# Optimization experiments

Measured on AMD Instinct MI355X. Metric: run time of the kernel, lower is better.

Reference implementation:

```python
import jax, jax.numpy as jnp
import numpy as np

EPS = 1e-5


def _conv1x1(x, w, b):
    # x: (B,C,H,W), w: (O,C), b: (O,)
    return jnp.einsum('bchw,oc->bohw', x, w) + b[None, :, None, None]


def setup_inputs() -> dict:
    key = jax.random.key(0)
    ks = jax.random.split(key, 12)
    C, Ci = 512, 256
    B, H, W = 4, 64, 64
    s_in = 1.0 / np.sqrt(C)
    s_ci = 1.0 / np.sqrt(Ci)
    return {
        'x': jax.random.normal(ks[0], (B, C, H, W), dtype=jnp.float32),
        'g_w': jax.random.normal(ks[1], (Ci, C), dtype=jnp.float32) * s_in,
        'g_b': jax.random.normal(ks[2], (Ci,), dtype=jnp.float32) * 0.01,
        'theta_w': jax.random.normal(ks[3], (Ci, C), dtype=jnp.float32) * s_in,
        'theta_b': jax.random.normal(ks[4], (Ci,), dtype=jnp.float32) * 0.01,
        'phi_w': jax.random.normal(ks[5], (Ci, C), dtype=jnp.float32) * s_in,
        'phi_b': jax.random.normal(ks[6], (Ci,), dtype=jnp.float32) * 0.01,
        'W_w': jax.random.normal(ks[7], (C, Ci), dtype=jnp.float32) * s_ci,
        'W_b': jax.random.normal(ks[8], (C,), dtype=jnp.float32) * 0.01,
        'bn_gamma': jax.random.normal(ks[9], (C,), dtype=jnp.float32) * 0.1,
        'bn_beta': jax.random.normal(ks[10], (C,), dtype=jnp.float32) * 0.01,
    }


def reference(x, g_w, g_b, theta_w, theta_b, phi_w, phi_b, W_w, W_b, bn_gamma, bn_beta):
    B, C, H, W = x.shape
    Ci = g_w.shape[0]
    HW = H * W
    # 1x1-conv projections -> token form
    g = _conv1x1(x, g_w, g_b).reshape(B, Ci, HW).transpose(0, 2, 1)        # (B,HW,Ci)
    theta = _conv1x1(x, theta_w, theta_b).reshape(B, Ci, HW).transpose(0, 2, 1)  # (B,HW,Ci)
    phi = _conv1x1(x, phi_w, phi_b).reshape(B, Ci, HW)                      # (B,Ci,HW)
    # dense HWxHW attention, scaled by sqrt(inter_channels)
    pairwise = jnp.einsum('bnc,bcm->bnm', theta, phi) / jnp.sqrt(jnp.float32(Ci))
    attn = jax.nn.softmax(pairwise, axis=-1)
    y = jnp.einsum('bnm,bmc->bnc', attn, g)                                 # (B,HW,Ci)
    y = y.transpose(0, 2, 1).reshape(B, Ci, H, W)
    # output 1x1 conv + BatchNorm2d (training-mode batch statistics)
    z = _conv1x1(y, W_w, W_b)
    mean = jnp.mean(z, axis=(0, 2, 3), keepdims=True)
    var = jnp.var(z, axis=(0, 2, 3), keepdims=True)
    z = bn_gamma[None, :, None, None] * (z - mean) * jax.lax.rsqrt(var + EPS) + bn_beta[None, :, None, None]
    return z + x
```

## Files before the change

kernel.cpp:

```cpp
#include <hip/hip_runtime.h>

typedef unsigned short u16;
typedef __attribute__((ext_vector_type(4))) u16 u16x4;
typedef __attribute__((ext_vector_type(8))) u16 u16x8;
typedef __attribute__((ext_vector_type(8))) short s16x8;
typedef __attribute__((ext_vector_type(4))) float f32x4;
typedef __attribute__((ext_vector_type(16))) float f32x16;

#define B_  4
#define C_  512
#define CI_ 256
#define HW_ 4096

static __device__ __forceinline__ u16 f2bf(float f) {
  unsigned u = __float_as_uint(f);
  return (u16)((u + 0x7FFFu + ((u >> 16) & 1u)) >> 16);
}
static __device__ __forceinline__ float bf2f(u16 h) {
  return __uint_as_float(((unsigned)h) << 16);
}

static __device__ __forceinline__ f32x4 mfma16(s16x8 a, s16x8 b, f32x4 c) {
  return __builtin_amdgcn_mfma_f32_16x16x32_bf16(a, b, c, 0, 0, 0);
}
static __device__ __forceinline__ f32x16 mfma32(s16x8 a, s16x8 b, f32x16 c) {
  return __builtin_amdgcn_mfma_f32_32x32x16_bf16(a, b, c, 0, 0, 0);
}

typedef __attribute__((address_space(3))) unsigned int as3_u32;
typedef const __attribute__((address_space(1))) unsigned int as1_u32;
static __device__ __forceinline__ void gload16(const u16* g, u16* l) {
  __builtin_amdgcn_global_load_lds((as1_u32*)g, (as3_u32*)l, 16, 0, 0);
}

__global__ __launch_bounds__(256) void k0_wcvt(
    const float* __restrict__ wg, const float* __restrict__ wt,
    const float* __restrict__ wp, const float* __restrict__ Ww,
    u16* __restrict__ wB, u16* __restrict__ WwB)
{
  int idx = (blockIdx.x * 256 + threadIdx.x) * 8;
  const float* src;
  u16* dst;
  if (idx < 393216) {
    int r = idx >> 17;
    src = (r == 0 ? wg : r == 1 ? wt : wp) + (idx & 131071);
    dst = wB + idx;
  } else {
    src = Ww + (idx - 393216);
    dst = WwB + (idx - 393216);
  }
  float4 v0 = *reinterpret_cast<const float4*>(src);
  float4 v1 = *reinterpret_cast<const float4*>(src + 4);
  u16x8 h;
  h[0] = f2bf(v0.x); h[1] = f2bf(v0.y); h[2] = f2bf(v0.z); h[3] = f2bf(v0.w);
  h[4] = f2bf(v1.x); h[5] = f2bf(v1.y); h[6] = f2bf(v1.z); h[7] = f2bf(v1.w);
  *reinterpret_cast<u16x8*>(dst) = h;
}

__global__ __launch_bounds__(256) void k0_xt(
    const float* __restrict__ x, u16* __restrict__ xT, int b0)
{
  __shared__ u16 lds[64][72];
  const int tid = threadIdx.x;
  const int n0 = blockIdx.x * 64, c0 = blockIdx.y * 64;
  const int bl = blockIdx.z;
  const int b = b0 + bl;
  const int nc = (tid & 15) * 4;
#pragma unroll
  for (int i = 0; i < 4; ++i) {
    int cr = (tid >> 4) + i * 16;
    float4 v = *reinterpret_cast<const float4*>(
        &x[((size_t)(b * C_ + c0 + cr)) * HW_ + n0 + nc]);
    u16x4 h; h[0] = f2bf(v.x); h[1] = f2bf(v.y); h[2] = f2bf(v.z); h[3] = f2bf(v.w);
    *reinterpret_cast<u16x4*>(&lds[cr][nc]) = h;
  }
  __syncthreads();
  const int n = tid & 63, cg = tid >> 6;
  u16x8 o0, o1;
#pragma unroll
  for (int j = 0; j < 8; ++j) { o0[j] = lds[cg * 16 + j][n]; o1[j] = lds[cg * 16 + 8 + j][n]; }
  size_t dstb = ((size_t)bl * HW_ + n0 + n) * C_ + c0 + cg * 16;
  *reinterpret_cast<u16x8*>(&xT[dstb])     = o0;
  *reinterpret_cast<u16x8*>(&xT[dstb + 8]) = o1;
}

__global__ __launch_bounds__(256) void k1_proj(
    const u16* __restrict__ wB, const u16* __restrict__ xT,
    const float* __restrict__ bg, const float* __restrict__ bt, const float* __restrict__ bp,
    u16* __restrict__ g_s, u16* __restrict__ thetaT, u16* __restrict__ phiT, int half)
{
  extern __shared__ u16 sm1[];
  const int tid = threadIdx.x;
  const int lane = tid & 63, wid = tid >> 6;
  const int wm = wid >> 1, wn = wid & 1;
  const int l15 = lane & 15, g4 = lane >> 4;

  const int bid = blockIdx.x;
  const int r12 = bid % 12;
  const int nt = bid / 12;
  const int mt = r12 >> 1;
  const int bl = r12 & 1;
  const int b = half * 2 + bl;
  const int m0 = mt * 128, n0g = nt * 128;
  const int p = mt >> 1;

  const u16* xb = xT + (size_t)bl * HW_ * C_;

  const int srow = tid >> 2, sch = tid & 3;
  const u16* a_src = wB + (size_t)(m0 + srow) * C_ + sch * 8;
  const u16* b_src = xb + (size_t)(n0g + srow) * C_ + sch * 8;

  f32x4 acc[4][4] = {};

  auto stage1 = [&](int buf, int ks) {
    u16* d = sm1 + buf * 8192;
#pragma unroll
    for (int i = 0; i < 2; ++i) {
      gload16(a_src + (size_t)(i * 64) * C_ + ks * 32, d + (tid + i * 256) * 8);
      gload16(b_src + (size_t)(i * 64) * C_ + ks * 32, d + 4096 + (tid + i * 256) * 8);
    }
  };
  auto compute1 = [&](int buf) {
    const u16* A = sm1 + buf * 8192;
    const u16* Bt = A + 4096;
    s16x8 afr[4], bfr[4];
#pragma unroll
    for (int mf = 0; mf < 4; ++mf)
      afr[mf] = *reinterpret_cast<const s16x8*>(&A[(wm * 64 + mf * 16 + l15) * 32 + g4 * 8]);
#pragma unroll
    for (int nf = 0; nf < 4; ++nf)
      bfr[nf] = *reinterpret_cast<const s16x8*>(&Bt[(wn * 64 + nf * 16 + l15) * 32 + g4 * 8]);
#pragma unroll
    for (int mf = 0; mf < 4; ++mf)
#pragma unroll
      for (int nf = 0; nf < 4; ++nf)
        acc[mf][nf] = mfma16(afr[mf], bfr[nf], acc[mf][nf]);
  };

  stage1(0, 0); stage1(1, 1);
  int cur = 0;
#pragma unroll 1
  for (int ks = 0; ks < 15; ++ks) {
    asm volatile("s_waitcnt vmcnt(4)" ::: "memory");
    __builtin_amdgcn_s_barrier();
    compute1(cur);
    if (ks < 14) { int nb = cur + 2; if (nb >= 3) nb -= 3; stage1(nb, ks + 2); }
    cur = (cur == 2) ? 0 : cur + 1;
  }
  asm volatile("s_waitcnt vmcnt(0)" ::: "memory");
  __builtin_amdgcn_s_barrier();
  compute1(cur);
  __syncthreads();

  const float* bias = (p == 0) ? bg : (p == 1) ? bt : bp;
  const int cib = (mt & 1) * 128;
#pragma unroll
  for (int mf = 0; mf < 4; ++mf)
#pragma unroll
    for (int r = 0; r < 4; ++r) {
      float bv = bias[cib + wm * 64 + mf * 16 + g4 * 4 + r];
#pragma unroll
      for (int nf = 0; nf < 4; ++nf) acc[mf][nf][r] += bv;
    }

  if (p == 0) {
    u16* lds_t = sm1;
#pragma unroll
    for (int mf = 0; mf < 4; ++mf)
#pragma unroll
      for (int nf = 0; nf < 4; ++nf)
#pragma unroll
        for (int r = 0; r < 4; ++r)
          lds_t[(wm * 64 + mf * 16 + g4 * 4 + r) * 136 + wn * 64 + nf * 16 + l15] =
              f2bf(acc[mf][nf][r]);
    __syncthreads();
    const int m = tid >> 1, hh = tid & 1;
    size_t dst = ((size_t)b * CI_ + cib + m) * HW_ + n0g + hh * 64;
#pragma unroll
    for (int j = 0; j < 8; ++j)
      *reinterpret_cast<u16x8*>(&g_s[dst + j * 8]) =
          *reinterpret_cast<const u16x8*>(&lds_t[m * 136 + hh * 64 + j * 8]);
  } else {
    u16* outp = (p == 1) ? thetaT : phiT;
#pragma unroll
    for (int mf = 0; mf < 4; ++mf)
#pragma unroll
      for (int nf = 0; nf < 4; ++nf) {
        u16x4 h;
#pragma unroll
        for (int r = 0; r < 4; ++r) h[r] = f2bf(acc[mf][nf][r]);
        int n = n0g + wn * 64 + nf * 16 + l15;
        *reinterpret_cast<u16x4*>(
            &outp[((size_t)b * HW_ + n) * CI_ + cib + wm * 64 + mf * 16 + g4 * 4]) = h;
      }
  }
}

#define OFF_PHI  0
#define OFF_G    32768
#define OFF_P    65536
#define OFF_LP   73728

__global__ __launch_bounds__(512, 2) void k3_fused(
    const u16* __restrict__ thetaT, const u16* __restrict__ phiT,
    const u16* __restrict__ g_s, u16* __restrict__ y)
{
  extern __shared__ u16 smem[];
  float* Lp = (float*)(smem + OFF_LP);
  float* iL = Lp + 256;

  const int tid = threadIdx.x;
  const int lane = tid & 63, w = tid >> 6;
  const int l31 = lane & 31, h = lane >> 5;
  const int l15 = lane & 15;

  const int bid = blockIdx.x;
  const int xcd = bid & 7, slot = bid >> 3;
  const int b  = xcd >> 1;
  const int n0 = ((xcd & 1) * 32 + slot) * 64;

  const int mh = w >> 1, nh = w & 1;
  const int cq = w >> 1, nh2 = w & 1;

  const u16* thb = thetaT + (size_t)b * HW_ * CI_;
  const u16* phb = phiT   + (size_t)b * HW_ * CI_;
  const u16* gsb = g_s    + (size_t)b * CI_ * HW_;

  s16x8 thfr[16];
#pragma unroll
  for (int cs = 0; cs < 16; ++cs)
    thfr[cs] = *reinterpret_cast<const s16x8*>(
        &thb[(size_t)(n0 + nh * 32 + l31) * CI_ + cs * 16 + h * 8]);

  const int prow = tid >> 5, pj = tid & 31;
  const int grow = tid >> 4, gj = tid & 15;
  const u16* ph_src = phb + (size_t)prow * CI_ + ((pj ^ prow) * 8);
  const u16* g_src  = gsb + (size_t)grow * HW_ + ((gj ^ (grow & 15)) * 8);
  const int ph_do = prow * 256 + pj * 8;
  const int g_do  = grow * 128 + gj * 8;

  auto stage_phi = [&](int mt) {
#pragma unroll
    for (int i = 0; i < 8; ++i)
      gload16(ph_src + (size_t)(mt + i * 16) * CI_, smem + OFF_PHI + ph_do + i * 4096);
  };
  auto stage_g = [&](int mt) {
#pragma unroll
    for (int i = 0; i < 8; ++i)
      gload16(g_src + mt + (size_t)(i * 32) * HW_, smem + OFF_G + g_do + i * 4096);
  };

  f32x16 oacc[2] = {};
  float psum = 0.f;

  auto qk_it = [&]() {
    const u16* phc = smem + OFF_PHI;
    u16* pb = smem + OFF_P;
    f32x16 acc = {};
    __builtin_amdgcn_s_setprio(1);
#pragma unroll
    for (int cs = 0; cs < 16; ++cs) {
      s16x8 a = *reinterpret_cast<const s16x8*>(
          &phc[(mh * 32 + l31) * 256 + (((cs * 2 + h) ^ l15) * 8)]);
      acc = mfma32(a, thfr[cs], acc);
    }
    __builtin_amdgcn_s_setprio(0);
    const int nloc = nh * 32 + l31;
#pragma unroll
    for (int g = 0; g < 4; ++g) {
      u16x4 pk;
#pragma unroll
      for (int r = 0; r < 4; ++r) {
        float e = __expf(acc[4 * g + r] * 0.0625f);
        psum += e;
        pk[r] = f2bf(e);
      }
      *reinterpret_cast<u16x4*>(
          &pb[nloc * 128 + (((mh * 4 + g) ^ l15) * 8) + h * 4]) = pk;
    }
  };
  auto pv_it = [&]() {
    const u16* pb = smem + OFF_P;
    const u16* gC = smem + OFF_G;
    const int nloc = nh2 * 32 + l31;
    __builtin_amdgcn_s_setprio(1);
#pragma unroll
    for (int ks = 0; ks < 8; ++ks) {
      s16x8 pa = *reinterpret_cast<const s16x8*>(
          &pb[nloc * 128 + (((ks * 2 + h) ^ l15) * 8)]);
#pragma unroll
      for (int ct = 0; ct < 2; ++ct) {
        int c = cq * 64 + ct * 32 + l31;
        s16x8 gb = *reinterpret_cast<const s16x8*>(
            &gC[c * 128 + (((ks * 2 + h) ^ l15) * 8)]);
        oacc[ct] = mfma32(pa, gb, oacc[ct]);
      }
    }
    __builtin_amdgcn_s_setprio(0);
  };

  stage_phi(0);
  __syncthreads();

#pragma unroll 1
  for (int it = 0; it < 32; ++it) {
    stage_g(it * 128);
    qk_it();
    __syncthreads();
    if (it < 31) stage_phi((it + 1) * 128);
    pv_it();
    __syncthreads();
  }

  psum += __shfl_xor(psum, 32);
  if (lane < 32) Lp[w * 32 + lane] = psum;
  __syncthreads();
  if (tid < 64) {
    int nhh = tid >> 5, j = tid & 31;
    iL[tid] = 1.0f / (Lp[(0 * 2 + nhh) * 32 + j] + Lp[(1 * 2 + nhh) * 32 + j] +
                      Lp[(2 * 2 + nhh) * 32 + j] + Lp[(3 * 2 + nhh) * 32 + j]);
  }
  __syncthreads();

  u16* yb = y + ((size_t)b * HW_ + n0) * CI_;
#pragma unroll
  for (int ct = 0; ct < 2; ++ct) {
    int c = cq * 64 + ct * 32 + l31;
#pragma unroll
    for (int reg = 0; reg < 16; ++reg) {
      int nl = nh2 * 32 + (reg & 3) + 8 * (reg >> 2) + 4 * h;
      yb[(size_t)nl * CI_ + c] = f2bf(oacc[ct][reg] * iL[nl]);
    }
  }
}

__global__ __launch_bounds__(256) void k4_wconv(
    const u16* __restrict__ WwB, const u16* __restrict__ y, const float* __restrict__ Wb,
    u16* __restrict__ z, float* __restrict__ zsum, float* __restrict__ zsq)
{
  extern __shared__ u16 sm4[];
  __shared__ float lds_ps[2][128][2];
  const int tid = threadIdx.x;
  const int lane = tid & 63, wid = tid >> 6;
  const int wm = wid >> 1, wn = wid & 1;
  const int l15 = lane & 15, g4 = lane >> 4;

  const int bid = blockIdx.x;
  const int xcd = bid & 7, slot = bid >> 3;
  const int b = xcd >> 1, half = xcd & 1;
  const int mt = slot & 3;
  const int nt = half * 16 + (slot >> 2);
  const int o0 = mt * 128, n0g = nt * 128;

  const int srow = tid >> 2, sch = tid & 3;
  const u16* a_src = WwB + (size_t)(o0 + srow) * CI_ + sch * 8;
  const u16* b_src = y + ((size_t)(b * HW_ + n0g + srow)) * CI_ + sch * 8;

  f32x4 acc[4][4] = {};

  auto stage4 = [&](int buf, int ks) {
    u16* d = sm4 + buf * 8192;
#pragma unroll
    for (int i = 0; i < 2; ++i) {
      gload16(a_src + (size_t)(i * 64) * CI_ + ks * 32, d + (tid + i * 256) * 8);
      gload16(b_src + (size_t)(i * 64) * CI_ + ks * 32, d + 4096 + (tid + i * 256) * 8);
    }
  };
  auto compute4 = [&](int buf) {
    const u16* A = sm4 + buf * 8192;
    const u16* Bt = A + 4096;
    s16x8 afr[4], bfr[4];
#pragma unroll
    for (int mf = 0; mf < 4; ++mf)
      afr[mf] = *reinterpret_cast<const s16x8*>(&A[(wm * 64 + mf * 16 + l15) * 32 + g4 * 8]);
#pragma unroll
    for (int nf = 0; nf < 4; ++nf)
      bfr[nf] = *reinterpret_cast<const s16x8*>(&Bt[(wn * 64 + nf * 16 + l15) * 32 + g4 * 8]);
#pragma unroll
    for (int mf = 0; mf < 4; ++mf)
#pragma unroll
      for (int nf = 0; nf < 4; ++nf)
        acc[mf][nf] = mfma16(afr[mf], bfr[nf], acc[mf][nf]);
  };

  stage4(0, 0); stage4(1, 1);
  int cur = 0;
#pragma unroll 1
  for (int ks = 0; ks < 7; ++ks) {
    asm volatile("s_waitcnt vmcnt(4)" ::: "memory");
    __builtin_amdgcn_s_barrier();
    compute4(cur);
    if (ks < 6) { int nb = cur + 2; if (nb >= 3) nb -= 3; stage4(nb, ks + 2); }
    cur = (cur == 2) ? 0 : cur + 1;
  }
  asm volatile("s_waitcnt vmcnt(0)" ::: "memory");
  __builtin_amdgcn_s_barrier();
  compute4(cur);
  __syncthreads();

  u16* lds_t = sm4;
#pragma unroll
  for (int mf = 0; mf < 4; ++mf)
#pragma unroll
    for (int r = 0; r < 4; ++r) {
      const int ol = wm * 64 + mf * 16 + g4 * 4 + r;
      float wb = Wb[o0 + ol];
      float s = 0.f, q = 0.f;
#pragma unroll
      for (int nf = 0; nf < 4; ++nf) {
        float zv = acc[mf][nf][r] + wb;
        s += zv; q += zv * zv;
        lds_t[ol * 136 + wn * 64 + nf * 16 + l15] = f2bf(zv);
      }
      s += __shfl_xor(s, 1); s += __shfl_xor(s, 2); s += __shfl_xor(s, 4); s += __shfl_xor(s, 8);
      q += __shfl_xor(q, 1); q += __shfl_xor(q, 2); q += __shfl_xor(q, 4); q += __shfl_xor(q, 8);
      if (l15 == 0) { lds_ps[wn][ol][0] = s; lds_ps[wn][ol][1] = q; }
    }
  __syncthreads();
  {
    const int m = tid >> 1, hh = tid & 1;
    size_t dst = ((size_t)(b * C_ + o0 + m)) * HW_ + n0g + hh * 64;
#pragma unroll
    for (int j = 0; j < 8; ++j)
      *reinterpret_cast<u16x8*>(&z[dst + j * 8]) =
          *reinterpret_cast<const u16x8*>(&lds_t[m * 136 + hh * 64 + j * 8]);
  }
  if (tid < 128) {
    int col = b * 32 + nt;
    zsum[(size_t)(o0 + tid) * 128 + col] = lds_ps[0][tid][0] + lds_ps[1][tid][0];
    zsq [(size_t)(o0 + tid) * 128 + col] = lds_ps[0][tid][1] + lds_ps[1][tid][1];
  }
}

__global__ void k5_bnstat(const float* __restrict__ zsum, const float* __restrict__ zsq,
                          const float* __restrict__ gamma, const float* __restrict__ beta,
                          float* __restrict__ bns, float* __restrict__ bnb)
{
  int ch = blockIdx.x * 256 + threadIdx.x;
  if (ch >= C_) return;
  float s = 0.f, q = 0.f;
  for (int i = 0; i < 128; ++i) { s += zsum[(size_t)ch * 128 + i]; q += zsq[(size_t)ch * 128 + i]; }
  const float inv_n = 1.0f / (B_ * HW_);
  float mean = s * inv_n;
  float var  = q * inv_n - mean * mean;
  float sc = gamma[ch] * rsqrtf(var + 1e-5f);
  bns[ch] = sc;
  bnb[ch] = beta[ch] - mean * sc;
}

__global__ __launch_bounds__(256) void k6_final(
    const u16* __restrict__ z, const float* __restrict__ x,
    const float* __restrict__ bns, const float* __restrict__ bnb,
    float* __restrict__ out)
{
  size_t i = ((size_t)blockIdx.x * 256 + threadIdx.x) * 8;
  int ch = (int)((i >> 12) & 511);
  float sc = bns[ch], sh = bnb[ch];
  u16x8 zv = *reinterpret_cast<const u16x8*>(&z[i]);
  float4 x0 = *reinterpret_cast<const float4*>(&x[i]);
  float4 x1 = *reinterpret_cast<const float4*>(&x[i + 4]);
  float4 o0, o1;
  o0.x = bf2f(zv[0]) * sc + sh + x0.x;
  o0.y = bf2f(zv[1]) * sc + sh + x0.y;
  o0.z = bf2f(zv[2]) * sc + sh + x0.z;
  o0.w = bf2f(zv[3]) * sc + sh + x0.w;
  o1.x = bf2f(zv[4]) * sc + sh + x1.x;
  o1.y = bf2f(zv[5]) * sc + sh + x1.y;
  o1.z = bf2f(zv[6]) * sc + sh + x1.z;
  o1.w = bf2f(zv[7]) * sc + sh + x1.w;
  *reinterpret_cast<float4*>(&out[i])     = o0;
  *reinterpret_cast<float4*>(&out[i + 4]) = o1;
}

extern "C" void kernel_launch(void* const* d_in, const int* in_sizes, int n_in,
                              void* d_out, int out_size, void* d_ws, size_t ws_size,
                              hipStream_t stream)
{
  (void)in_sizes; (void)n_in; (void)out_size; (void)ws_size;
  const float* x    = (const float*)d_in[0];
  const float* g_w  = (const float*)d_in[1];
  const float* g_b  = (const float*)d_in[2];
  const float* t_w  = (const float*)d_in[3];
  const float* t_b  = (const float*)d_in[4];
  const float* p_w  = (const float*)d_in[5];
  const float* p_b  = (const float*)d_in[6];
  const float* W_w  = (const float*)d_in[7];
  const float* W_b  = (const float*)d_in[8];
  const float* bng  = (const float*)d_in[9];
  const float* bnb_ = (const float*)d_in[10];

  char* ws = (char*)d_ws;
  const size_t M8 = (size_t)8 << 20;
  u16*   xT     = (u16*)(ws + 0);
  u16*   y      = (u16*)(ws + 0);
  u16*   thetaT = (u16*)(ws + M8);
  u16*   phiT   = (u16*)(ws + 2 * M8);
  u16*   g_s    = (u16*)(ws + 3 * M8);
  u16*   zbf    = (u16*)(ws + M8);
  float* zsum   = (float*)(ws + 3 * M8);
  float* zsq    = (float*)(ws + 3 * M8 + 262144);
  float* bnsV   = (float*)(ws + 3 * M8 + 524288);
  float* bnbV   = (float*)(ws + 3 * M8 + 526336);
  u16*   wB     = (u16*)(ws + 4 * M8);
  u16*   WwB    = (u16*)(ws + 4 * M8 + 786432);
  float* out    = (float*)d_out;

  const int k1_lds = 49152;
  const int k3_lds = 148736;
  const int k4_lds = 49152;
  hipFuncSetAttribute(reinterpret_cast<const void*>(k1_proj),
                      hipFuncAttributeMaxDynamicSharedMemorySize, k1_lds);
  hipFuncSetAttribute(reinterpret_cast<const void*>(k3_fused),
                      hipFuncAttributeMaxDynamicSharedMemorySize, k3_lds);
  hipFuncSetAttribute(reinterpret_cast<const void*>(k4_wconv),
                      hipFuncAttributeMaxDynamicSharedMemorySize, k4_lds);

  hipLaunchKernelGGL(k0_wcvt, dim3(256), dim3(256), 0, stream,
                     g_w, t_w, p_w, W_w, wB, WwB);
  for (int half = 0; half < 2; ++half) {
    hipLaunchKernelGGL(k0_xt, dim3(64, 8, 2), dim3(256), 0, stream, x, xT, half * 2);
    hipLaunchKernelGGL(k1_proj, dim3(384), dim3(256), k1_lds, stream,
                       wB, xT, g_b, t_b, p_b, g_s, thetaT, phiT, half);
  }
  hipLaunchKernelGGL(k3_fused, dim3(256), dim3(512), k3_lds, stream,
                     thetaT, phiT, g_s, y);
  hipLaunchKernelGGL(k4_wconv, dim3(512), dim3(256), k4_lds, stream,
                     WwB, y, W_b, zbf, zsum, zsq);
  hipLaunchKernelGGL(k5_bnstat, dim3(2), dim3(256), 0, stream,
                     zsum, zsq, bng, bnb_, bnsV, bnbV);
  hipLaunchKernelGGL(k6_final, dim3(4096), dim3(256), 0, stream,
                     zbf, x, bnsV, bnbV, out);
}
```

Before: 187.5 us.

## Keep softmax probabilities in registers and split PV over key slices

The attention kernel no longer writes exp-scores to an LDS P buffer for the PV matmul. Each wave packs its own QK accumulator into MFMA A-operands using lane shuffles. It then multiplies them against all 256 output channels for its slice of keys, which requires 8 f32x16 accumulators per wave. A serialized four-step LDS reduction across the key-slice waves follows, then vectorized bf16 stores. This removes the P write/read round-trip and a sync dependency, at the cost of much higher register pressure and an extra reduction phase.

```diff
diff --git a/kernel.cpp b/kernel.cpp
--- a/kernel.cpp
+++ b/kernel.cpp
@@ -6,6 +6,7 @@
 typedef __attribute__((ext_vector_type(8))) short s16x8;
 typedef __attribute__((ext_vector_type(4))) float f32x4;
 typedef __attribute__((ext_vector_type(16))) float f32x16;
+typedef __attribute__((ext_vector_type(4))) unsigned u32x4;
 
 #define B_  4
 #define C_  512
@@ -198,15 +199,14 @@
 
 #define OFF_PHI  0
 #define OFF_G    32768
-#define OFF_P    65536
-#define OFF_LP   73728
+#define OFF_LPW  65536
 
 __global__ __launch_bounds__(512, 2) void k3_fused(
     const u16* __restrict__ thetaT, const u16* __restrict__ phiT,
     const u16* __restrict__ g_s, u16* __restrict__ y)
 {
   extern __shared__ u16 smem[];
-  float* Lp = (float*)(smem + OFF_LP);
+  float* Lp = (float*)(smem + OFF_LPW);
   float* iL = Lp + 256;
 
   const int tid = threadIdx.x;
@@ -220,7 +220,6 @@
   const int n0 = ((xcd & 1) * 32 + slot) * 64;
 
   const int mh = w >> 1, nh = w & 1;
-  const int cq = w >> 1, nh2 = w & 1;
 
   const u16* thb = thetaT + (size_t)b * HW_ * CI_;
   const u16* phb = phiT   + (size_t)b * HW_ * CI_;
@@ -250,12 +249,12 @@
       gload16(g_src + mt + (size_t)(i * 32) * HW_, smem + OFF_G + g_do + i * 4096);
   };
 
-  f32x16 oacc[2] = {};
+  f32x16 oacc[8] = {};
   float psum = 0.f;
+  s16x8 pa0, pa1;
 
   auto qk_it = [&]() {
     const u16* phc = smem + OFF_PHI;
-    u16* pb = smem + OFF_P;
     f32x16 acc = {};
     __builtin_amdgcn_s_setprio(1);
 #pragma unroll
@@ -265,34 +264,50 @@
       acc = mfma32(a, thfr[cs], acc);
     }
     __builtin_amdgcn_s_setprio(0);
-    const int nloc = nh * 32 + l31;
-#pragma unroll
-    for (int g = 0; g < 4; ++g) {
-      u16x4 pk;
-#pragma unroll
-      for (int r = 0; r < 4; ++r) {
-        float e = __expf(acc[4 * g + r] * 0.0625f);
-        psum += e;
-        pk[r] = f2bf(e);
-      }
-      *reinterpret_cast<u16x4*>(
-          &pb[nloc * 128 + (((mh * 4 + g) ^ l15) * 8) + h * 4]) = pk;
-    }
-  };
+    float p[16];
+#pragma unroll
+    for (int r = 0; r < 16; ++r) {
+      p[r] = __expf(acc[r] * 0.0625f);
+      psum += p[r];
+    }
+    unsigned q[4][2];
+#pragma unroll
+    for (int qi = 0; qi < 4; ++qi) {
+      q[qi][0] = ((unsigned)f2bf(p[4 * qi + 1]) << 16) | f2bf(p[4 * qi]);
+      q[qi][1] = ((unsigned)f2bf(p[4 * qi + 3]) << 16) | f2bf(p[4 * qi + 2]);
+    }
+    unsigned sa0 = h ? q[0][0] : q[1][0];
+    unsigned sa1 = h ? q[0][1] : q[1][1];
+    unsigned sb0 = h ? q[2][0] : q[3][0];
+    unsigned sb1 = h ? q[2][1] : q[3][1];
+    unsigned ra0 = __shfl_xor(sa0, 32);
+    unsigned ra1 = __shfl_xor(sa1, 32);
+    unsigned rb0 = __shfl_xor(sb0, 32);
+    unsigned rb1 = __shfl_xor(sb1, 32);
+    u32x4 w0, w1;
+    w0[0] = h ? ra0 : q[0][0];
+    w0[1] = h ? ra1 : q[0][1];
+    w0[2] = h ? q[1][0] : ra0;
+    w0[3] = h ? q[1][1] : ra1;
+    w1[0] = h ? rb0 : q[2][0];
+    w1[1] = h ? rb1 : q[2][1];
+    w1[2] = h ? q[3][0] : rb0;
+    w1[3] = h ? q[3][1] : rb1;
+    pa0 = *reinterpret_cast<s16x8*>(&w0);
+    pa1 = *reinterpret_cast<s16x8*>(&w1);
+  };
+
   auto pv_it = [&]() {
-    const u16* pb = smem + OFF_P;
     const u16* gC = smem + OFF_G;
-    const int nloc = nh2 * 32 + l31;
     __builtin_amdgcn_s_setprio(1);
 #pragma unroll
-    for (int ks = 0; ks < 8; ++ks) {
-      s16x8 pa = *reinterpret_cast<const s16x8*>(
-          &pb[nloc * 128 + (((ks * 2 + h) ^ l15) * 8)]);
-#pragma unroll
-      for (int ct = 0; ct < 2; ++ct) {
-        int c = cq * 64 + ct * 32 + l31;
+    for (int ks = 0; ks < 2; ++ks) {
+      s16x8 pa = ks ? pa1 : pa0;
+      const int chunk = mh * 4 + ks * 2 + h;
+#pragma unroll
+      for (int ct = 0; ct < 8; ++ct) {
         s16x8 gb = *reinterpret_cast<const s16x8*>(
-            &gC[c * 128 + (((ks * 2 + h) ^ l15) * 8)]);
+            &gC[(ct * 32 + l31) * 128 + ((chunk ^ l15) * 8)]);
         oacc[ct] = mfma32(pa, gb, oacc[ct]);
       }
     }
@@ -322,14 +337,37 @@
   }
   __syncthreads();
 
+  float* ored = (float*)smem;
+#pragma unroll 1
+  for (int step = 0; step < 4; ++step) {
+    if (mh == step) {
+#pragma unroll
+      for (int ct = 0; ct < 8; ++ct)
+#pragma unroll
+        for (int reg = 0; reg < 16; ++reg) {
+          int n = nh * 32 + (reg & 3) + 8 * (reg >> 2) + 4 * h;
+          int c = ct * 32 + l31;
+          if (step == 0) ored[n * 260 + c] = oacc[ct][reg];
+          else           ored[n * 260 + c] += oacc[ct][reg];
+        }
+    }
+    __syncthreads();
+  }
+
   u16* yb = y + ((size_t)b * HW_ + n0) * CI_;
-#pragma unroll
-  for (int ct = 0; ct < 2; ++ct) {
-    int c = cq * 64 + ct * 32 + l31;
-#pragma unroll
-    for (int reg = 0; reg < 16; ++reg) {
-      int nl = nh2 * 32 + (reg & 3) + 8 * (reg >> 2) + 4 * h;
-      yb[(size_t)nl * CI_ + c] = f2bf(oacc[ct][reg] * iL[nl]);
+  {
+    const int n = tid >> 3, cc = (tid & 7) * 32;
+    float il = iL[n];
+#pragma unroll
+    for (int jj = 0; jj < 4; ++jj) {
+      f32x4 v0 = *reinterpret_cast<const f32x4*>(&ored[n * 260 + cc + jj * 8]);
+      f32x4 v1 = *reinterpret_cast<const f32x4*>(&ored[n * 260 + cc + jj * 8 + 4]);
+      u16x8 o;
+      o[0] = f2bf(v0[0] * il); o[1] = f2bf(v0[1] * il);
+      o[2] = f2bf(v0[2] * il); o[3] = f2bf(v0[3] * il);
+      o[4] = f2bf(v1[0] * il); o[5] = f2bf(v1[1] * il);
+      o[6] = f2bf(v1[2] * il); o[7] = f2bf(v1[3] * il);
+      *reinterpret_cast<u16x8*>(&yb[(size_t)n * CI_ + cc + jj * 8]) = o;
     }
   }
 }
@@ -506,7 +544,7 @@
   float* out    = (float*)d_out;
 
   const int k1_lds = 49152;
-  const int k3_lds = 148736;
+  const int k3_lds = 132352;
   const int k4_lds = 49152;
   hipFuncSetAttribute(reinterpret_cast<const void*>(k1_proj),
                       hipFuncAttributeMaxDynamicSharedMemorySize, k1_lds);
```

Result: slower. 229.5 us (+22.4%).

## Load full-K tiles for output conv at once with swizzled LDS and 32x32 MFMA

Applied to the files above, without the earlier changes.

The output 1x1 conv kernel now loads the whole K=256 slice of both operand tiles into LDS in one shot, using an XOR-swizzled layout, then runs 32x32x16 MFMAs with no per-step barriers. This replaces the triple-buffered K-loop of 16x16 MFMAs and is meant to cut barrier and pipeline overhead and LDS bank conflicts. The cost is 128KB of LDS per block, which limits occupancy to one block per CU and gives up overlap of loads with compute. The BN partial-sum reductions are adapted to the 32-lane layout.

```diff
diff --git a/kernel.cpp b/kernel.cpp
--- a/kernel.cpp
+++ b/kernel.cpp
@@ -334,87 +334,83 @@
   }
 }
 
-__global__ __launch_bounds__(256) void k4_wconv(
+#define K4_A 0
+#define K4_B 32768
+
+__global__ __launch_bounds__(256, 1) void k4_wconv(
     const u16* __restrict__ WwB, const u16* __restrict__ y, const float* __restrict__ Wb,
     u16* __restrict__ z, float* __restrict__ zsum, float* __restrict__ zsq)
 {
   extern __shared__ u16 sm4[];
   __shared__ float lds_ps[2][128][2];
   const int tid = threadIdx.x;
-  const int lane = tid & 63, wid = tid >> 6;
-  const int wm = wid >> 1, wn = wid & 1;
-  const int l15 = lane & 15, g4 = lane >> 4;
+  const int lane = tid & 63, w = tid >> 6;
+  const int wo = w >> 1, wn2 = w & 1;
+  const int l31 = lane & 31, h = lane >> 5;
+  const int l15 = lane & 15;
 
   const int bid = blockIdx.x;
   const int xcd = bid & 7, slot = bid >> 3;
-  const int b = xcd >> 1, half = xcd & 1;
+  const int b = xcd >> 1, halfq = xcd & 1;
   const int mt = slot & 3;
-  const int nt = half * 16 + (slot >> 2);
+  const int nt = halfq * 16 + (slot >> 2);
   const int o0 = mt * 128, n0g = nt * 128;
 
-  const int srow = tid >> 2, sch = tid & 3;
-  const u16* a_src = WwB + (size_t)(o0 + srow) * CI_ + sch * 8;
-  const u16* b_src = y + ((size_t)(b * HW_ + n0g + srow)) * CI_ + sch * 8;
-
-  f32x4 acc[4][4] = {};
-
-  auto stage4 = [&](int buf, int ks) {
-    u16* d = sm4 + buf * 8192;
-#pragma unroll
-    for (int i = 0; i < 2; ++i) {
-      gload16(a_src + (size_t)(i * 64) * CI_ + ks * 32, d + (tid + i * 256) * 8);
-      gload16(b_src + (size_t)(i * 64) * CI_ + ks * 32, d + 4096 + (tid + i * 256) * 8);
-    }
-  };
-  auto compute4 = [&](int buf) {
-    const u16* A = sm4 + buf * 8192;
-    const u16* Bt = A + 4096;
-    s16x8 afr[4], bfr[4];
-#pragma unroll
-    for (int mf = 0; mf < 4; ++mf)
-      afr[mf] = *reinterpret_cast<const s16x8*>(&A[(wm * 64 + mf * 16 + l15) * 32 + g4 * 8]);
-#pragma unroll
-    for (int nf = 0; nf < 4; ++nf)
-      bfr[nf] = *reinterpret_cast<const s16x8*>(&Bt[(wn * 64 + nf * 16 + l15) * 32 + g4 * 8]);
-#pragma unroll
-    for (int mf = 0; mf < 4; ++mf)
-#pragma unroll
-      for (int nf = 0; nf < 4; ++nf)
-        acc[mf][nf] = mfma16(afr[mf], bfr[nf], acc[mf][nf]);
-  };
-
-  stage4(0, 0); stage4(1, 1);
-  int cur = 0;
-#pragma unroll 1
-  for (int ks = 0; ks < 7; ++ks) {
-    asm volatile("s_waitcnt vmcnt(4)" ::: "memory");
-    __builtin_amdgcn_s_barrier();
-    compute4(cur);
-    if (ks < 6) { int nb = cur + 2; if (nb >= 3) nb -= 3; stage4(nb, ks + 2); }
-    cur = (cur == 2) ? 0 : cur + 1;
-  }
-  asm volatile("s_waitcnt vmcnt(0)" ::: "memory");
-  __builtin_amdgcn_s_barrier();
-  compute4(cur);
+  const int prow = tid >> 5, pj = tid & 31;
+  const u16* aE = WwB + (size_t)(o0 + prow) * CI_ + ((pj ^ prow) * 8);
+  const u16* aO = WwB + (size_t)(o0 + prow) * CI_ + ((pj ^ prow ^ 8) * 8);
+  const u16* bE = y + ((size_t)(b * HW_ + n0g + prow)) * CI_ + ((pj ^ prow) * 8);
+  const u16* bO = y + ((size_t)(b * HW_ + n0g + prow)) * CI_ + ((pj ^ prow ^ 8) * 8);
+  const int s_do = prow * 256 + pj * 8;
+
+#pragma unroll
+  for (int i = 0; i < 16; ++i) {
+    const u16* sa = (i & 1) ? aO : aE;
+    const u16* sb = (i & 1) ? bO : bE;
+    gload16(sa + (size_t)(i * 8) * CI_, sm4 + K4_A + s_do + i * 2048);
+    gload16(sb + (size_t)(i * 8) * CI_, sm4 + K4_B + s_do + i * 2048);
+  }
+  __syncthreads();
+
+  f32x16 acc[2][2] = {};
+  {
+    const u16* A = sm4 + K4_A;
+    const u16* Bt = sm4 + K4_B;
+#pragma unroll
+    for (int cs = 0; cs < 16; ++cs) {
+      s16x8 a0 = *reinterpret_cast<const s16x8*>(
+          &A[(wo * 64 + 0 + l31) * 256 + (((cs * 2 + h) ^ l15) * 8)]);
+      s16x8 a1 = *reinterpret_cast<const s16x8*>(
+          &A[(wo * 64 + 32 + l31) * 256 + (((cs * 2 + h) ^ l15) * 8)]);
+      s16x8 b0 = *reinterpret_cast<const s16x8*>(
+          &Bt[(wn2 * 64 + 0 + l31) * 256 + (((cs * 2 + h) ^ l15) * 8)]);
+      s16x8 b1 = *reinterpret_cast<const s16x8*>(
+          &Bt[(wn2 * 64 + 32 + l31) * 256 + (((cs * 2 + h) ^ l15) * 8)]);
+      acc[0][0] = mfma32(a0, b0, acc[0][0]);
+      acc[0][1] = mfma32(a0, b1, acc[0][1]);
+      acc[1][0] = mfma32(a1, b0, acc[1][0]);
+      acc[1][1] = mfma32(a1, b1, acc[1][1]);
+    }
+  }
   __syncthreads();
 
   u16* lds_t = sm4;
 #pragma unroll
-  for (int mf = 0; mf < 4; ++mf)
-#pragma unroll
-    for (int r = 0; r < 4; ++r) {
-      const int ol = wm * 64 + mf * 16 + g4 * 4 + r;
+  for (int ot = 0; ot < 2; ++ot)
+#pragma unroll
+    for (int reg = 0; reg < 16; ++reg) {
+      const int ol = wo * 64 + ot * 32 + (reg & 3) + 8 * (reg >> 2) + 4 * h;
       float wb = Wb[o0 + ol];
-      float s = 0.f, q = 0.f;
-#pragma unroll
-      for (int nf = 0; nf < 4; ++nf) {
-        float zv = acc[mf][nf][r] + wb;
-        s += zv; q += zv * zv;
-        lds_t[ol * 136 + wn * 64 + nf * 16 + l15] = f2bf(zv);
-      }
-      s += __shfl_xor(s, 1); s += __shfl_xor(s, 2); s += __shfl_xor(s, 4); s += __shfl_xor(s, 8);
-      q += __shfl_xor(q, 1); q += __shfl_xor(q, 2); q += __shfl_xor(q, 4); q += __shfl_xor(q, 8);
-      if (l15 == 0) { lds_ps[wn][ol][0] = s; lds_ps[wn][ol][1] = q; }
+      float z0 = acc[ot][0][reg] + wb;
+      float z1 = acc[ot][1][reg] + wb;
+      lds_t[ol * 136 + wn2 * 64 + l31]      = f2bf(z0);
+      lds_t[ol * 136 + wn2 * 64 + 32 + l31] = f2bf(z1);
+      float s = z0 + z1, q = z0 * z0 + z1 * z1;
+      s += __shfl_xor(s, 1); s += __shfl_xor(s, 2); s += __shfl_xor(s, 4);
+      s += __shfl_xor(s, 8); s += __shfl_xor(s, 16);
+      q += __shfl_xor(q, 1); q += __shfl_xor(q, 2); q += __shfl_xor(q, 4);
+      q += __shfl_xor(q, 8); q += __shfl_xor(q, 16);
+      if (l31 == 0) { lds_ps[wn2][ol][0] = s; lds_ps[wn2][ol][1] = q; }
     }
   __syncthreads();
   {
@@ -507,7 +503,7 @@
 
   const int k1_lds = 49152;
   const int k3_lds = 148736;
-  const int k4_lds = 49152;
+  const int k4_lds = 131072;
   hipFuncSetAttribute(reinterpret_cast<const void*>(k1_proj),
                       hipFuncAttributeMaxDynamicSharedMemorySize, k1_lds);
   hipFuncSetAttribute(reinterpret_cast<const void*>(k3_fused),
```

Result: slower. 197.9 us (+5.6%).
